# Optimization experiments

Hardware: AMD Instinct MI355X
Metric: run time of the kernel (lower is better)

The kernel has to match this reference:

```python
import jax, jax.numpy as jnp
import numpy as np

HID = 128; L = 4; N = 100000; E = 1600000; B = 512; OUT = 1
NVOC = 101; EVOC = 21

def layer_norm(x, g, b, eps=1e-5):
    m = x.mean(-1, keepdims=True)
    v = ((x - m) ** 2).mean(-1, keepdims=True)
    return (x - m) * jax.lax.rsqrt(v + eps) * g + b

def setup_inputs() -> dict:
    key = jax.random.key(0)
    ks = jax.random.split(key, 20)
    s = 1.0 / np.sqrt(HID)
    return {
        "x_idx": jax.random.randint(ks[0], (N,), 0, NVOC),
        "edge_index": jax.random.randint(ks[1], (2, E), 0, N),
        "edge_attr": jax.random.randint(ks[2], (E, 3), 0, EVOC),
        "batch": jnp.sort(jax.random.randint(ks[3], (N,), 0, B)),
        "node_emb": jax.random.normal(ks[4], (NVOC, HID), jnp.float32) * 0.02,
        "e1": jax.random.normal(ks[5], (EVOC, HID), jnp.float32) * 0.02,
        "e2": jax.random.normal(ks[6], (EVOC, HID), jnp.float32) * 0.02,
        "e3": jax.random.normal(ks[7], (EVOC, HID), jnp.float32) * 0.02,
        "W1": jax.random.normal(ks[8], (L, HID, HID), jnp.float32) * s,
        "b1": jnp.zeros((L, HID), jnp.float32),
        "W2": jax.random.normal(ks[9], (L, HID, HID), jnp.float32) * s,
        "b2": jnp.zeros((L, HID), jnp.float32),
        "ln_g": jnp.ones((L, HID), jnp.float32),
        "ln_b": jnp.zeros((L, HID), jnp.float32),
        "pW1": jax.random.normal(ks[10], (HID, HID), jnp.float32) * s,
        "pb1": jnp.zeros((HID,), jnp.float32),
        "pW2": jax.random.normal(ks[11], (HID, HID), jnp.float32) * s,
        "pb2": jnp.zeros((HID,), jnp.float32),
        "pg": jnp.ones((HID,), jnp.float32),
        "pbn": jnp.zeros((HID,), jnp.float32),
        "oW": jax.random.normal(ks[12], (HID, OUT), jnp.float32) * s,
        "ob": jnp.zeros((OUT,), jnp.float32),
    }

def reference(x_idx, edge_index, edge_attr, batch, node_emb, e1, e2, e3,
              W1, b1, W2, b2, ln_g, ln_b, pW1, pb1, pW2, pb2, pg, pbn, oW, ob):
    # input embedding (inmlp) and bond embedding (edge_emb1+2+3)
    x = node_emb[x_idx]                                   # [N, H]
    bond = e1[edge_attr[:, 0]] + e2[edge_attr[:, 1]] + e3[edge_attr[:, 2]]  # [E, H]
    src, dst = edge_index[0], edge_index[1]
    # residual GINEConv stack: x = x + nn((1+eps)*x + sum_j relu(x_j + bond))
    for l in range(L):
        msg = jax.nn.relu(x[src] + bond)                  # gather + fuse
        agg = jax.ops.segment_sum(msg, dst, num_segments=N)  # scatter-add
        h = x + agg                                       # eps = 0
        h = jax.nn.relu(h @ W1[l] + b1[l])
        h = h @ W2[l] + b2[l]
        h = jax.nn.relu(layer_norm(h, ln_g[l], ln_b[l]))
        x = x + h
    # node-level mean pool per graph (node_pool='mean')
    sums = jax.ops.segment_sum(x, batch, num_segments=B)  # [B, H]
    cnt = jax.ops.segment_sum(jnp.ones((N, 1), x.dtype), batch, num_segments=B)
    g = sums / jnp.maximum(cnt, 1.0)
    h = jax.nn.relu(g @ pW1 + pb1)
    h = h @ pW2 + pb2
    h = jax.nn.relu(layer_norm(h, pg, pbn))
    return jax.nn.sigmoid(h @ oW + ob)                    # [B, 1]
```

## Files before the change

### kernel.cpp

```cpp
#include <hip/hip_runtime.h>

#define HID 128
#define NN  100000
#define EE  1600000
#define BB  512
#define LL  4
#define FROWS 16

typedef __attribute__((ext_vector_type(8))) short bf16x8;
typedef __attribute__((ext_vector_type(4))) float f32x4;

__device__ __forceinline__ unsigned short f32_to_bf16(float f) {
    union { float f; unsigned u; } c; c.f = f;
    unsigned r = c.u + 0x7FFFu + ((c.u >> 16) & 1u);
    return (unsigned short)(r >> 16);
}
__device__ __forceinline__ float bf16_to_f32(unsigned short h) {
    union { unsigned u; float f; } c; c.u = ((unsigned)h) << 16; return c.f;
}

__global__ __launch_bounds__(256) void hist_kernel(
    const int* __restrict__ ei, int* __restrict__ R)
{
    int e = blockIdx.x * 256 + threadIdx.x;
    if (e >= EE) return;
    atomicAdd(&R[ei[EE + e] + 1], 1);
}

__global__ __launch_bounds__(256) void scan1_kernel(int* __restrict__ R,
                                                    int* __restrict__ aux, int n)
{
    __shared__ int sh[256];
    int base = blockIdx.x * 1024;
    int t = threadIdx.x;
    int v[4]; int s = 0;
#pragma unroll
    for (int i = 0; i < 4; ++i) {
        int idx = base + t * 4 + i;
        v[i] = (idx < n) ? R[idx] : 0;
        s += v[i];
    }
    sh[t] = s; __syncthreads();
#pragma unroll
    for (int off = 1; off < 256; off <<= 1) {
        int val = (t >= off) ? sh[t - off] : 0;
        __syncthreads();
        sh[t] += val;
        __syncthreads();
    }
    int run = (t == 0) ? 0 : sh[t - 1];
#pragma unroll
    for (int i = 0; i < 4; ++i) {
        int idx = base + t * 4 + i;
        run += v[i];
        if (idx < n) R[idx] = run;
    }
    if (t == 255) aux[blockIdx.x] = sh[255];
}

__global__ __launch_bounds__(128) void scan2_kernel(int* __restrict__ aux, int nb)
{
    __shared__ int sh[128];
    int t = threadIdx.x;
    sh[t] = (t < nb) ? aux[t] : 0;
    __syncthreads();
#pragma unroll
    for (int off = 1; off < 128; off <<= 1) {
        int val = (t >= off) ? sh[t - off] : 0;
        __syncthreads();
        sh[t] += val;
        __syncthreads();
    }
    if (t < nb) aux[t] = sh[t];
}

__global__ __launch_bounds__(256) void scan3_kernel(int* __restrict__ R,
                                                    const int* __restrict__ aux, int n)
{
    int b = blockIdx.x + 1;
    int add = aux[b - 1];
#pragma unroll
    for (int i = 0; i < 4; ++i) {
        int idx = b * 1024 + threadIdx.x * 4 + i;
        if (idx < n) R[idx] += add;
    }
}

__global__ __launch_bounds__(256) void fill_kernel(
    const int* __restrict__ ei, const int* __restrict__ ea,
    int* __restrict__ R, unsigned int* __restrict__ csr)
{
    int e = blockIdx.x * 256 + threadIdx.x;
    if (e >= EE) return;
    int pos = atomicAdd(&R[ei[EE + e]], 1);
    unsigned int rec = (unsigned int)ei[e]
                     | ((unsigned int)ea[e * 3 + 0] << 17)
                     | ((unsigned int)ea[e * 3 + 1] << 22)
                     | ((unsigned int)ea[e * 3 + 2] << 27);
    csr[pos] = rec;
}

__global__ __launch_bounds__(256) void embed_kernel(
    const int* __restrict__ x_idx, const float* __restrict__ node_emb,
    float* __restrict__ x)
{
    int t = blockIdx.x * 256 + threadIdx.x;
    int node = t >> 5, j = t & 31;
    if (node >= NN) return;
    ((float4*)x)[node * 32 + j] =
        ((const float4*)node_emb)[x_idx[node] * 32 + j];
}

__global__ __launch_bounds__(256) void wprep_kernel(
    const float* __restrict__ W1, const float* __restrict__ W2,
    unsigned short* __restrict__ wf)
{
    int t = blockIdx.x * 256 + threadIdx.x;
    if (t >= LL * 2 * 16384) return;
    int layer = t >> 15;
    int rem = t & 32767;
    int mat = rem >> 14;
    int idx = rem & 16383;
    int k = idx >> 7, n = idx & 127;
    const float* W = (mat ? W2 : W1) + layer * 16384;
    float w = W[k * 128 + n];
    unsigned short hi = f32_to_bf16(w);
    unsigned short lo = f32_to_bf16(w - bf16_to_f32(hi));
    int nb = n >> 4, nl = n & 15, kstep = k >> 5, quad = (k >> 3) & 3, j = k & 7;
    int di = ((nb * 4 + kstep) * 64 + (quad * 16 + nl)) * 8 + j;
    unsigned short* base = wf + (size_t)((layer * 2 + mat) * 2) * 16384;
    base[di] = hi;
    base[16384 + di] = lo;
}

__device__ __forceinline__ float4 edge_term(
    unsigned int rec, int l32, const float* __restrict__ x,
    const float* __restrict__ e1, const float* __restrict__ e2,
    const float* __restrict__ e3)
{
    int src = rec & 0x1FFFF;
    int i0 = (rec >> 17) & 31, i1 = (rec >> 22) & 31, i2 = (rec >> 27) & 31;
    float4 v  = ((const float4*)x )[src * 32 + l32];
    float4 w1 = ((const float4*)e1)[i0  * 32 + l32];
    float4 w2 = ((const float4*)e2)[i1  * 32 + l32];
    float4 w3 = ((const float4*)e3)[i2  * 32 + l32];
    float4 r;
    r.x = fmaxf(v.x + w1.x + w2.x + w3.x, 0.f);
    r.y = fmaxf(v.y + w1.y + w2.y + w3.y, 0.f);
    r.z = fmaxf(v.z + w1.z + w2.z + w3.z, 0.f);
    r.w = fmaxf(v.w + w1.w + w2.w + w3.w, 0.f);
    return r;
}

#define TPAD 136
#define UPAD 132

__global__ __launch_bounds__(256) void layer_fused_kernel(
    const float* __restrict__ xin,
    const float* __restrict__ e1, const float* __restrict__ e2,
    const float* __restrict__ e3,
    const int* __restrict__ rowend, const unsigned int* __restrict__ csr,
    const unsigned short* __restrict__ wf,
    const float* __restrict__ b1, const float* __restrict__ b2,
    const float* __restrict__ gamma, const float* __restrict__ beta,
    float* __restrict__ xout)
{
    __shared__ __align__(16) char smemA[8704];
    __shared__ __align__(16) unsigned short t_hi[FROWS * TPAD];
    __shared__ __align__(16) unsigned short t_lo[FROWS * TPAD];
    unsigned short* h_hi = (unsigned short*)smemA;
    unsigned short* h_lo = (unsigned short*)(smemA + 4352);
    float* u_s = (float*)smemA;

    int tid = threadIdx.x;
    int rbase = blockIdx.x * FROWS;
    int w = tid >> 6;
    int lane = tid & 63;
    int half = lane >> 5;
    int l32  = lane & 31;

    for (int ln = w * 4; ln < w * 4 + 4; ++ln) {
        int node = rbase + ln;
        int beg = (node == 0) ? 0 : rowend[node - 1];
        int end = rowend[node];

        float4 a0 = make_float4(0.f, 0.f, 0.f, 0.f);
        float4 a1 = make_float4(0.f, 0.f, 0.f, 0.f);
        float4 a2 = make_float4(0.f, 0.f, 0.f, 0.f);
        float4 a3 = make_float4(0.f, 0.f, 0.f, 0.f);
        int p = beg + half;
        for (; p + 6 < end; p += 8) {
            unsigned int r0 = csr[p];
            unsigned int r1 = csr[p + 2];
            unsigned int r2 = csr[p + 4];
            unsigned int r3 = csr[p + 6];
            float4 t0 = edge_term(r0, l32, xin, e1, e2, e3);
            float4 t1 = edge_term(r1, l32, xin, e1, e2, e3);
            float4 t2 = edge_term(r2, l32, xin, e1, e2, e3);
            float4 t3 = edge_term(r3, l32, xin, e1, e2, e3);
            a0.x += t0.x; a0.y += t0.y; a0.z += t0.z; a0.w += t0.w;
            a1.x += t1.x; a1.y += t1.y; a1.z += t1.z; a1.w += t1.w;
            a2.x += t2.x; a2.y += t2.y; a2.z += t2.z; a2.w += t2.w;
            a3.x += t3.x; a3.y += t3.y; a3.z += t3.z; a3.w += t3.w;
        }
        for (; p < end; p += 2) {
            float4 t0 = edge_term(csr[p], l32, xin, e1, e2, e3);
            a0.x += t0.x; a0.y += t0.y; a0.z += t0.z; a0.w += t0.w;
        }
        float4 acc;
        acc.x = (a0.x + a1.x) + (a2.x + a3.x);
        acc.y = (a0.y + a1.y) + (a2.y + a3.y);
        acc.z = (a0.z + a1.z) + (a2.z + a3.z);
        acc.w = (a0.w + a1.w) + (a2.w + a3.w);
        acc.x += __shfl_xor(acc.x, 32);
        acc.y += __shfl_xor(acc.y, 32);
        acc.z += __shfl_xor(acc.z, 32);
        acc.w += __shfl_xor(acc.w, 32);
        if (half == 0) {
            float4 xv = ((const float4*)xin)[node * 32 + l32];
            float h0 = xv.x + acc.x, h1 = xv.y + acc.y;
            float h2 = xv.z + acc.z, h3 = xv.w + acc.w;
            unsigned short i0 = f32_to_bf16(h0), i1 = f32_to_bf16(h1);
            unsigned short i2 = f32_to_bf16(h2), i3 = f32_to_bf16(h3);
            int o = ln * TPAD + l32 * 4;
            *(ushort4*)&h_hi[o] = make_ushort4(i0, i1, i2, i3);
            *(ushort4*)&h_lo[o] =
                make_ushort4(f32_to_bf16(h0 - bf16_to_f32(i0)),
                             f32_to_bf16(h1 - bf16_to_f32(i1)),
                             f32_to_bf16(h2 - bf16_to_f32(i2)),
                             f32_to_bf16(h3 - bf16_to_f32(i3)));
        }
    }
    __syncthreads();

    int quad = lane >> 4, nl = lane & 15;
    int cbg = w * 2;
    const unsigned short* w1_hi = wf;
    const unsigned short* w1_lo = wf + 16384;
    const unsigned short* w2_hi = wf + 32768;
    const unsigned short* w2_lo = wf + 49152;

    {
        f32x4 acc[2] = {};
#pragma unroll
        for (int ks = 0; ks < 4; ++ks) {
            int koff = ks * 32 + quad * 8;
            bf16x8 a_hi = *(const bf16x8*)&h_hi[nl * TPAD + koff];
            bf16x8 a_lo = *(const bf16x8*)&h_lo[nl * TPAD + koff];
#pragma unroll
            for (int cb = 0; cb < 2; ++cb) {
                int off = (((cbg + cb) * 4 + ks) * 64 + lane) * 8;
                bf16x8 b_hi = *(const bf16x8*)&w1_hi[off];
                bf16x8 b_lo = *(const bf16x8*)&w1_lo[off];
                acc[cb] = __builtin_amdgcn_mfma_f32_16x16x32_bf16(a_hi, b_hi, acc[cb], 0, 0, 0);
                acc[cb] = __builtin_amdgcn_mfma_f32_16x16x32_bf16(a_lo, b_hi, acc[cb], 0, 0, 0);
                acc[cb] = __builtin_amdgcn_mfma_f32_16x16x32_bf16(a_hi, b_lo, acc[cb], 0, 0, 0);
            }
        }
#pragma unroll
        for (int cb = 0; cb < 2; ++cb) {
            int col = (cbg + cb) * 16 + nl;
            float bv = b1[col];
#pragma unroll
            for (int r = 0; r < 4; ++r) {
                int row = quad * 4 + r;
                float v = fmaxf(acc[cb][r] + bv, 0.f);
                unsigned short hi = f32_to_bf16(v);
                t_hi[row * TPAD + col] = hi;
                t_lo[row * TPAD + col] = f32_to_bf16(v - bf16_to_f32(hi));
            }
        }
    }
    __syncthreads();

    {
        f32x4 acc[2] = {};
#pragma unroll
        for (int ks = 0; ks < 4; ++ks) {
            int koff = ks * 32 + quad * 8;
            bf16x8 a_hi = *(const bf16x8*)&t_hi[nl * TPAD + koff];
            bf16x8 a_lo = *(const bf16x8*)&t_lo[nl * TPAD + koff];
#pragma unroll
            for (int cb = 0; cb < 2; ++cb) {
                int off = (((cbg + cb) * 4 + ks) * 64 + lane) * 8;
                bf16x8 b_hi = *(const bf16x8*)&w2_hi[off];
                bf16x8 b_lo = *(const bf16x8*)&w2_lo[off];
                acc[cb] = __builtin_amdgcn_mfma_f32_16x16x32_bf16(a_hi, b_hi, acc[cb], 0, 0, 0);
                acc[cb] = __builtin_amdgcn_mfma_f32_16x16x32_bf16(a_lo, b_hi, acc[cb], 0, 0, 0);
                acc[cb] = __builtin_amdgcn_mfma_f32_16x16x32_bf16(a_hi, b_lo, acc[cb], 0, 0, 0);
            }
        }
#pragma unroll
        for (int cb = 0; cb < 2; ++cb) {
            int col = (cbg + cb) * 16 + nl;
            float bv = b2[col];
#pragma unroll
            for (int r = 0; r < 4; ++r) {
                int row = quad * 4 + r;
                u_s[row * UPAD + col] = acc[cb][r] + bv;
            }
        }
    }
    __syncthreads();

    {
        int tc = tid & 31, tr = tid >> 5;
        float4 gv  = ((const float4*)gamma)[tc];
        float4 btv = ((const float4*)beta )[tc];
#pragma unroll
        for (int j = 0; j < 2; ++j) {
            int row = tr * 2 + j;
            float4 u4 = *(const float4*)&u_s[row * UPAD + tc * 4];
            float s = u4.x + u4.y + u4.z + u4.w;
            float q = u4.x*u4.x + u4.y*u4.y + u4.z*u4.z + u4.w*u4.w;
#pragma unroll
            for (int off = 1; off < 32; off <<= 1) {
                s += __shfl_xor(s, off, 64);
                q += __shfl_xor(q, off, 64);
            }
            float m   = s * (1.f / 128.f);
            float var = q * (1.f / 128.f) - m * m;
            float rs  = rsqrtf(var + 1e-5f);
            int g = rbase + row;
            float4 xo = ((const float4*)xin)[g * 32 + tc];
            float4 o;
            o.x = xo.x + fmaxf((u4.x - m) * rs * gv.x + btv.x, 0.f);
            o.y = xo.y + fmaxf((u4.y - m) * rs * gv.y + btv.y, 0.f);
            o.z = xo.z + fmaxf((u4.z - m) * rs * gv.z + btv.z, 0.f);
            o.w = xo.w + fmaxf((u4.w - m) * rs * gv.w + btv.w, 0.f);
            ((float4*)xout)[g * 32 + tc] = o;
        }
    }
}

__global__ __launch_bounds__(256) void edge_kernel(
    const float* __restrict__ x, const int* __restrict__ ei,
    const int* __restrict__ ea, const float* __restrict__ e1,
    const float* __restrict__ e2, const float* __restrict__ e3,
    float* __restrict__ agg)
{
    int t = blockIdx.x * 256 + threadIdx.x;
    int e = t >> 5, j = t & 31;
    if (e >= EE) return;
    int src = ei[e];
    int dst = ei[EE + e];
    int a0 = ea[e * 3 + 0], a1 = ea[e * 3 + 1], a2 = ea[e * 3 + 2];
    float4 v  = ((const float4*)x )[src * 32 + j];
    float4 w1 = ((const float4*)e1)[a0  * 32 + j];
    float4 w2 = ((const float4*)e2)[a1  * 32 + j];
    float4 w3 = ((const float4*)e3)[a2  * 32 + j];
    float mx = fmaxf(v.x + w1.x + w2.x + w3.x, 0.f);
    float my = fmaxf(v.y + w1.y + w2.y + w3.y, 0.f);
    float mz = fmaxf(v.z + w1.z + w2.z + w3.z, 0.f);
    float mw = fmaxf(v.w + w1.w + w2.w + w3.w, 0.f);
    float* ag = agg + (size_t)dst * HID + j * 4;
    atomicAdd(ag + 0, mx);
    atomicAdd(ag + 1, my);
    atomicAdd(ag + 2, mz);
    atomicAdd(ag + 3, mw);
}

__global__ __launch_bounds__(256) void gemm_relu_kernel(
    const float* __restrict__ x, const float* __restrict__ agg,
    const float* __restrict__ W, const float* __restrict__ bias,
    float* __restrict__ t)
{
    __shared__ float h_s[32 * 129];
    int tid = threadIdx.x;
    int tc = tid & 31, tr = tid >> 5;
    int rbase = blockIdx.x * 32;
    for (int idx = tid; idx < 32 * 128; idx += 256) {
        int r = idx >> 7, k = idx & 127;
        int g = (rbase + r) * HID + k;
        h_s[r * 129 + k] = x[g] + agg[g];
    }
    __syncthreads();
    float acc[4][4] = {};
    const float4* W4 = (const float4*)W;
#pragma unroll 4
    for (int k = 0; k < 128; ++k) {
        float4 w = W4[k * 32 + tc];
#pragma unroll
        for (int j = 0; j < 4; ++j) {
            float hv = h_s[(tr * 4 + j) * 129 + k];
            acc[j][0] = fmaf(hv, w.x, acc[j][0]);
            acc[j][1] = fmaf(hv, w.y, acc[j][1]);
            acc[j][2] = fmaf(hv, w.z, acc[j][2]);
            acc[j][3] = fmaf(hv, w.w, acc[j][3]);
        }
    }
    float4 bv = ((const float4*)bias)[tc];
#pragma unroll
    for (int j = 0; j < 4; ++j) {
        int r = rbase + tr * 4 + j;
        float4 o;
        o.x = fmaxf(acc[j][0] + bv.x, 0.f);
        o.y = fmaxf(acc[j][1] + bv.y, 0.f);
        o.z = fmaxf(acc[j][2] + bv.z, 0.f);
        o.w = fmaxf(acc[j][3] + bv.w, 0.f);
        ((float4*)t)[r * 32 + tc] = o;
    }
}

__global__ __launch_bounds__(256) void gemm_ln_res_kernel(
    const float* __restrict__ t, const float* __restrict__ W,
    const float* __restrict__ bias, const float* __restrict__ gamma,
    const float* __restrict__ beta, float* __restrict__ x)
{
    __shared__ float h_s[32 * 129];
    int tid = threadIdx.x;
    int tc = tid & 31, tr = tid >> 5;
    int rbase = blockIdx.x * 32;
    for (int idx = tid; idx < 32 * 128; idx += 256) {
        int r = idx >> 7, k = idx & 127;
        h_s[r * 129 + k] = t[(rbase + r) * HID + k];
    }
    __syncthreads();
    float acc[4][4] = {};
    const float4* W4 = (const float4*)W;
#pragma unroll 4
    for (int k = 0; k < 128; ++k) {
        float4 w = W4[k * 32 + tc];
#pragma unroll
        for (int j = 0; j < 4; ++j) {
            float hv = h_s[(tr * 4 + j) * 129 + k];
            acc[j][0] = fmaf(hv, w.x, acc[j][0]);
            acc[j][1] = fmaf(hv, w.y, acc[j][1]);
            acc[j][2] = fmaf(hv, w.z, acc[j][2]);
            acc[j][3] = fmaf(hv, w.w, acc[j][3]);
        }
    }
    float4 bv  = ((const float4*)bias )[tc];
    float4 gv  = ((const float4*)gamma)[tc];
    float4 btv = ((const float4*)beta )[tc];
#pragma unroll
    for (int j = 0; j < 4; ++j) {
        acc[j][0] += bv.x; acc[j][1] += bv.y;
        acc[j][2] += bv.z; acc[j][3] += bv.w;
        float s = acc[j][0] + acc[j][1] + acc[j][2] + acc[j][3];
        float q = acc[j][0]*acc[j][0] + acc[j][1]*acc[j][1]
                + acc[j][2]*acc[j][2] + acc[j][3]*acc[j][3];
#pragma unroll
        for (int off = 1; off < 32; off <<= 1) {
            s += __shfl_xor(s, off, 64);
            q += __shfl_xor(q, off, 64);
        }
        float m   = s * (1.f / 128.f);
        float var = q * (1.f / 128.f) - m * m;
        float rs  = rsqrtf(var + 1e-5f);
        int r = rbase + tr * 4 + j;
        float4 xo = ((float4*)x)[r * 32 + tc];
        float4 o;
        o.x = xo.x + fmaxf((acc[j][0] - m) * rs * gv.x + btv.x, 0.f);
        o.y = xo.y + fmaxf((acc[j][1] - m) * rs * gv.y + btv.y, 0.f);
        o.z = xo.z + fmaxf((acc[j][2] - m) * rs * gv.z + btv.z, 0.f);
        o.w = xo.w + fmaxf((acc[j][3] - m) * rs * gv.w + btv.w, 0.f);
        ((float4*)x)[r * 32 + tc] = o;
    }
}

#define PCHUNK 32
__global__ __launch_bounds__(256) void pool_kernel(
    const float* __restrict__ x, const int* __restrict__ batch,
    float* __restrict__ sums, int* __restrict__ cnt)
{
    int wave = (blockIdx.x * 256 + threadIdx.x) >> 6;
    int lane = threadIdx.x & 63;
    int n0 = wave * PCHUNK;
    if (n0 >= NN) return;
    int n1 = n0 + PCHUNK; if (n1 > NN) n1 = NN;

    float2 acc = make_float2(0.f, 0.f);
    int cur = batch[n0];
    int run = 0;
    for (int n = n0; n < n1; ++n) {
        int b = batch[n];
        if (b != cur) {
            float* sp = sums + cur * HID + lane * 2;
            atomicAdd(sp + 0, acc.x);
            atomicAdd(sp + 1, acc.y);
            if (lane == 0) atomicAdd(&cnt[cur], run);
            acc = make_float2(0.f, 0.f);
            run = 0; cur = b;
        }
        float2 v = ((const float2*)x)[(size_t)n * 64 + lane];
        acc.x += v.x; acc.y += v.y; ++run;
    }
    float* sp = sums + cur * HID + lane * 2;
    atomicAdd(sp + 0, acc.x);
    atomicAdd(sp + 1, acc.y);
    if (lane == 0) atomicAdd(&cnt[cur], run);
}

__global__ __launch_bounds__(128) void head_kernel(
    const float* __restrict__ sums, const int* __restrict__ cnt,
    const float* __restrict__ pW1, const float* __restrict__ pb1,
    const float* __restrict__ pW2, const float* __restrict__ pb2,
    const float* __restrict__ pg, const float* __restrict__ pbn,
    const float* __restrict__ oW, const float* __restrict__ ob,
    float* __restrict__ out)
{
    __shared__ float s0[128], s1[128], red[4];
    int b = blockIdx.x, c = threadIdx.x;

    float cn = fmaxf((float)cnt[b], 1.f);
    s0[c] = sums[b * HID + c] / cn;
    __syncthreads();

    float a = pb1[c];
#pragma unroll 4
    for (int k = 0; k < HID; ++k) a = fmaf(s0[k], pW1[k * HID + c], a);
    a = fmaxf(a, 0.f);
    s1[c] = a;
    __syncthreads();

    float u = pb2[c];
#pragma unroll 4
    for (int k = 0; k < HID; ++k) u = fmaf(s1[k], pW2[k * HID + c], u);

    float s = u, q = u * u;
#pragma unroll
    for (int off = 1; off < 64; off <<= 1) {
        s += __shfl_xor(s, off, 64);
        q += __shfl_xor(q, off, 64);
    }
    if ((c & 63) == 0) { red[(c >> 6) * 2] = s; red[(c >> 6) * 2 + 1] = q; }
    __syncthreads();
    float S = red[0] + red[2], Q = red[1] + red[3];
    float m = S * (1.f / 128.f);
    float var = Q * (1.f / 128.f) - m * m;
    float rs = rsqrtf(var + 1e-5f);
    float v = fmaxf((u - m) * rs * pg[c] + pbn[c], 0.f);

    float p = v * oW[c];
#pragma unroll
    for (int off = 1; off < 64; off <<= 1) p += __shfl_xor(p, off, 64);
    __syncthreads();
    if ((c & 63) == 0) red[c >> 6] = p;
    __syncthreads();
    if (c == 0) {
        float tot = red[0] + red[1] + ob[0];
        out[b] = 1.f / (1.f + expf(-tot));
    }
}

extern "C" void kernel_launch(void* const* d_in, const int* in_sizes, int n_in,
                              void* d_out, int out_size, void* d_ws, size_t ws_size,
                              hipStream_t stream)
{
    const int*   x_idx    = (const int*)d_in[0];
    const int*   ei       = (const int*)d_in[1];
    const int*   ea       = (const int*)d_in[2];
    const int*   batch    = (const int*)d_in[3];
    const float* node_emb = (const float*)d_in[4];
    const float* e1       = (const float*)d_in[5];
    const float* e2       = (const float*)d_in[6];
    const float* e3       = (const float*)d_in[7];
    const float* W1       = (const float*)d_in[8];
    const float* b1       = (const float*)d_in[9];
    const float* W2       = (const float*)d_in[10];
    const float* b2       = (const float*)d_in[11];
    const float* lg       = (const float*)d_in[12];
    const float* lb       = (const float*)d_in[13];
    const float* pW1      = (const float*)d_in[14];
    const float* pb1      = (const float*)d_in[15];
    const float* pW2      = (const float*)d_in[16];
    const float* pb2      = (const float*)d_in[17];
    const float* pg       = (const float*)d_in[18];
    const float* pbn      = (const float*)d_in[19];
    const float* oW       = (const float*)d_in[20];
    const float* ob       = (const float*)d_in[21];
    float* out = (float*)d_out;

    char* base = (char*)d_ws;
    size_t Sx = (size_t)NN * HID * sizeof(float);
    float* x0   = (float*)(base);
    float* x1   = (float*)(base + Sx);
    float* sums = (float*)(base + 2 * Sx);
    int*   cnt  = (int*)  (base + 2 * Sx + BB * HID * 4);
    int*   R    = (int*)  (base + 2 * Sx + BB * HID * 4 + 2048);
    unsigned int* csr = (unsigned int*)((char*)R + 400016);
    int*   aux  = (int*)  ((char*)csr + (size_t)EE * 4);
    unsigned short* wf = (unsigned short*)((char*)aux + 512);
    size_t need = ((char*)wf + (size_t)LL * 2 * 2 * 16384 * 2) - base;

    bool fast = (ws_size >= need);

    embed_kernel<<<(NN * 32 + 255) / 256, 256, 0, stream>>>(x_idx, node_emb, x0);

    if (fast) {
        const int n = NN + 1, NB = (n + 1023) / 1024;
        hipMemsetAsync(R, 0, (size_t)n * sizeof(int), stream);
        hist_kernel <<<(EE + 255) / 256, 256, 0, stream>>>(ei, R);
        scan1_kernel<<<NB, 256, 0, stream>>>(R, aux, n);
        scan2_kernel<<<1, 128, 0, stream>>>(aux, NB);
        scan3_kernel<<<NB - 1, 256, 0, stream>>>(R, aux, n);
        fill_kernel <<<(EE + 255) / 256, 256, 0, stream>>>(ei, ea, R, csr);
        wprep_kernel<<<(LL * 2 * 16384 + 255) / 256, 256, 0, stream>>>(W1, W2, wf);

        for (int l = 0; l < LL; ++l) {
            const float* xin = (l & 1) ? x1 : x0;
            float*       xo  = (l & 1) ? x0 : x1;
            layer_fused_kernel<<<NN / FROWS, 256, 0, stream>>>(
                xin, e1, e2, e3, R, csr, wf + (size_t)l * 65536,
                b1 + l * HID, b2 + l * HID,
                lg + l * HID, lb + l * HID, xo);
        }
    } else {
        float* x   = x0;
        float* agg = x1;
        for (int l = 0; l < LL; ++l) {
            hipMemsetAsync(agg, 0, Sx, stream);
            edge_kernel<<<(EE * 32 + 255) / 256, 256, 0, stream>>>(
                x, ei, ea, e1, e2, e3, agg);
            gemm_relu_kernel<<<NN / 32, 256, 0, stream>>>(
                x, agg, W1 + l * HID * HID, b1 + l * HID, agg);
            gemm_ln_res_kernel<<<NN / 32, 256, 0, stream>>>(
                agg, W2 + l * HID * HID, b2 + l * HID,
                lg + l * HID, lb + l * HID, x);
        }
    }

    hipMemsetAsync(sums, 0,
                   (size_t)BB * HID * sizeof(float) + BB * sizeof(int), stream);
    {
        int waves = (NN + PCHUNK - 1) / PCHUNK;
        int blocks = (waves + 3) / 4;
        pool_kernel<<<blocks, 256, 0, stream>>>(x0, batch, sums, cnt);
    }
    head_kernel<<<BB, 128, 0, stream>>>(
        sums, cnt, pW1, pb1, pW2, pb2, pg, pbn, oW, ob, out);
}
```

Baseline: 1.085 ms.

## Process nodes in degree-sorted order to balance per-block edge work

Adds a counting sort of nodes by in-degree (histogram, suffix scan, scatter into a permutation), placing high-degree nodes first. The fused layer kernel then handles nodes through this permutation, so the nodes sharing a block and its waves have similar edge counts. The aim is to cut idle time from waves waiting on a neighbour with a long edge list. The cost is three extra small preprocessing kernels, plus scattered rather than contiguous row reads and writes in the epilogue.

Result: slower. 1.706 ms (+57.2%).

```diff
diff --git a/kernel.cpp b/kernel.cpp
--- a/kernel.cpp
+++ b/kernel.cpp
@@ -98,6 +98,39 @@
                      | ((unsigned int)ea[e * 3 + 1] << 22)
                      | ((unsigned int)ea[e * 3 + 2] << 27);
     csr[pos] = rec;
+}
+
+__global__ __launch_bounds__(256) void dhist_kernel(
+    const int* __restrict__ R, int* __restrict__ dbin)
+{
+    int n = blockIdx.x * 256 + threadIdx.x;
+    if (n >= NN) return;
+    int d = R[n] - (n ? R[n - 1] : 0);
+    if (d > 255) d = 255;
+    atomicAdd(&dbin[d], 1);
+}
+
+__global__ __launch_bounds__(256) void dscan_kernel(
+    const int* __restrict__ dbin, int* __restrict__ dstart)
+{
+    __shared__ int sh[256];
+    int t = threadIdx.x;
+    sh[t] = dbin[t];
+    __syncthreads();
+    int s = 0;
+    for (int e = t + 1; e < 256; ++e) s += sh[e];
+    dstart[t] = s;
+}
+
+__global__ __launch_bounds__(256) void dscatter_kernel(
+    const int* __restrict__ R, int* __restrict__ dstart, int* __restrict__ perm)
+{
+    int n = blockIdx.x * 256 + threadIdx.x;
+    if (n >= NN) return;
+    int d = R[n] - (n ? R[n - 1] : 0);
+    if (d > 255) d = 255;
+    int pos = atomicAdd(&dstart[d], 1);
+    perm[pos] = n;
 }
 
 __global__ __launch_bounds__(256) void embed_kernel(
@@ -160,6 +193,7 @@
     const float* __restrict__ e1, const float* __restrict__ e2,
     const float* __restrict__ e3,
     const int* __restrict__ rowend, const unsigned int* __restrict__ csr,
+    const int* __restrict__ perm,
     const unsigned short* __restrict__ wf,
     const float* __restrict__ b1, const float* __restrict__ b2,
     const float* __restrict__ gamma, const float* __restrict__ beta,
@@ -180,7 +214,7 @@
     int l32  = lane & 31;
 
     for (int ln = w * 4; ln < w * 4 + 4; ++ln) {
-        int node = rbase + ln;
+        int node = perm[rbase + ln];
         int beg = (node == 0) ? 0 : rowend[node - 1];
         int end = rowend[node];
 
@@ -321,7 +355,7 @@
             float m   = s * (1.f / 128.f);
             float var = q * (1.f / 128.f) - m * m;
             float rs  = rsqrtf(var + 1e-5f);
-            int g = rbase + row;
+            int g = perm[rbase + row];
             float4 xo = ((const float4*)xin)[g * 32 + tc];
             float4 o;
             o.x = xo.x + fmaxf((u4.x - m) * rs * gv.x + btv.x, 0.f);
@@ -582,7 +616,11 @@
     unsigned int* csr = (unsigned int*)((char*)R + 400016);
     int*   aux  = (int*)  ((char*)csr + (size_t)EE * 4);
     unsigned short* wf = (unsigned short*)((char*)aux + 512);
-    size_t need = ((char*)wf + (size_t)LL * 2 * 2 * 16384 * 2) - base;
+    char*  wf_end = (char*)wf + (size_t)LL * 2 * 2 * 16384 * 2;
+    int*   perm   = (int*)wf_end;
+    int*   dbin   = (int*)(wf_end + (size_t)NN * 4);
+    int*   dstart = dbin + 256;
+    size_t need = ((char*)(dstart + 256)) - base;
 
     bool fast = (ws_size >= need);
 
@@ -591,18 +629,22 @@
     if (fast) {
         const int n = NN + 1, NB = (n + 1023) / 1024;
         hipMemsetAsync(R, 0, (size_t)n * sizeof(int), stream);
+        hipMemsetAsync(dbin, 0, 256 * sizeof(int), stream);
         hist_kernel <<<(EE + 255) / 256, 256, 0, stream>>>(ei, R);
         scan1_kernel<<<NB, 256, 0, stream>>>(R, aux, n);
         scan2_kernel<<<1, 128, 0, stream>>>(aux, NB);
         scan3_kernel<<<NB - 1, 256, 0, stream>>>(R, aux, n);
         fill_kernel <<<(EE + 255) / 256, 256, 0, stream>>>(ei, ea, R, csr);
+        dhist_kernel<<<(NN + 255) / 256, 256, 0, stream>>>(R, dbin);
+        dscan_kernel<<<1, 256, 0, stream>>>(dbin, dstart);
+        dscatter_kernel<<<(NN + 255) / 256, 256, 0, stream>>>(R, dstart, perm);
         wprep_kernel<<<(LL * 2 * 16384 + 255) / 256, 256, 0, stream>>>(W1, W2, wf);
 
         for (int l = 0; l < LL; ++l) {
             const float* xin = (l & 1) ? x1 : x0;
             float*       xo  = (l & 1) ? x0 : x1;
             layer_fused_kernel<<<NN / FROWS, 256, 0, stream>>>(
-                xin, e1, e2, e3, R, csr, wf + (size_t)l * 65536,
+                xin, e1, e2, e3, R, csr, perm, wf + (size_t)l * 65536,
                 b1 + l * HID, b2 + l * HID,
                 lg + l * HID, lb + l * HID, xo);
         }
```
